# Performance work log

Measured on AMD Instinct MI355X. Metric: run time of the kernel, lower is better.

Reference implementation:

```python
import math
import jax, jax.numpy as jnp
import numpy as np

RATIO = 0.5
N_CHANNELS = 64
B = 64
N_PER = 8192  # nodes per batch element (equal counts for a regular reference)
D_POS = 3


def setup_inputs() -> dict:
    key = jax.random.key(0)
    k1, k2, k3 = jax.random.split(key, 3)
    N = B * N_PER
    positions = jax.random.normal(k1, (N, D_POS), dtype=jnp.float32)
    weights = jax.random.normal(k2, (N, N_CHANNELS), dtype=jnp.float32)
    w = jax.random.normal(k3, (N_CHANNELS,), dtype=jnp.float32)  # SelectTopK learnable vector
    batch = jnp.full((B,), N_PER, dtype=jnp.int32)  # per-batch-element node counts
    return {"positions": positions, "weights": weights, "w": w, "batch": batch}


def reference(positions, weights, w, batch):
    # SelectTopK: score = tanh((x @ w) / ||w||), then per-batch top-ceil(ratio*n) selection.
    n_b = batch.shape[0]
    n_per = positions.shape[0] // n_b
    k = int(math.ceil(RATIO * n_per))

    score = jnp.tanh((weights @ w) / jnp.linalg.norm(w))          # [N]
    top_vals, top_idx = jax.lax.top_k(score.reshape(n_b, n_per), k)  # [B,k] each

    # global node indices of selected nodes (descending score within each batch element)
    node_index = (top_idx + jnp.arange(n_b, dtype=top_idx.dtype)[:, None] * n_per).reshape(-1)  # [B*k]

    pos_sel = positions[node_index]                               # [B*k, D_POS]
    w_sel = weights[node_index] * top_vals.reshape(-1)[:, None]   # [B*k, C] gated by score
    # histc recount: each batch element keeps exactly k nodes
    new_batch = jnp.full((n_b,), k, dtype=jnp.int32)
    return pos_sel, w_sel, new_batch
```

## Files before the change

kernel.cpp:

```cpp
#include <hip/hip_runtime.h>
#include <math.h>

#define C 64
#define DPOS 3
#define NPER 8192
#define KK 4096
#define IDX_MASK 0x1FFFULL

typedef unsigned long long ull;

__device__ __forceinline__ ull score_key(double s, unsigned idx) {
    ull u = (ull)__double_as_longlong(s);
    ull o = (u >> 63) ? ~u : (u | 0x8000000000000000ULL);
    ull d = ~o;
    return (d & ~IDX_MASK) | (ull)idx;
}

__device__ __forceinline__ float key_to_score(ull key) {
    ull o = ~key;
    ull u = (o >> 63) ? (o & 0x7FFFFFFFFFFFFFFFULL) : ~o;
    u &= ~IDX_MASK;
    return (float)__longlong_as_double((long long)u);
}

__global__ void score_kernel(const float* __restrict__ weights,
                             const float* __restrict__ w,
                             ull* __restrict__ keys, int n) {
    int wid = (blockIdx.x * blockDim.x + threadIdx.x) >> 6;
    int lane = threadIdx.x & 63;
    int c4 = lane & 15;
    float4 wv = ((const float4*)w)[c4];
    double nrm = (double)wv.x * wv.x + (double)wv.y * wv.y +
                 (double)wv.z * wv.z + (double)wv.w * wv.w;
    #pragma unroll
    for (int off = 8; off >= 1; off >>= 1) nrm += __shfl_xor(nrm, off, 16);
    double sq = sqrt(nrm);
    #pragma unroll
    for (int it = 0; it < 4; ++it) {
        int r = wid * 16 + it * 4 + (lane >> 4);
        if (r >= n) return;
        float4 x = ((const float4*)weights)[(size_t)r * 16 + c4];
        double acc = (double)x.x * wv.x + (double)x.y * wv.y +
                     (double)x.z * wv.z + (double)x.w * wv.w;
        #pragma unroll
        for (int off = 8; off >= 1; off >>= 1) acc += __shfl_xor(acc, off, 16);
        double s = tanh(acc / sq);
        if (c4 == 0) keys[r] = score_key(s, (unsigned)(r & (NPER - 1)));
    }
}

#define CH 1024
#define CTH 128
__global__ __launch_bounds__(CTH) void sort_chunk(ull* __restrict__ keys) {
    __shared__ ull lds[CH];
    const int tid = threadIdx.x;
    ull* bk = keys + (size_t)blockIdx.x * CH;
    #pragma unroll
    for (int s = 0; s < CH / CTH; ++s) lds[tid + s * CTH] = bk[tid + s * CTH];
    for (unsigned k = 2; k <= CH; k <<= 1) {
        for (unsigned j = k >> 1; j > 0; j >>= 1) {
            __syncthreads();
            #pragma unroll
            for (int s = 0; s < CH / CTH; ++s) {
                unsigned i = tid + s * CTH;
                unsigned ixj = i ^ j;
                if (ixj > i) {
                    ull a = lds[i], b = lds[ixj];
                    bool up = ((i & k) == 0);
                    if ((a > b) == up) { lds[i] = b; lds[ixj] = a; }
                }
            }
        }
    }
    __syncthreads();
    #pragma unroll
    for (int s = 0; s < CH / CTH; ++s) bk[tid + s * CTH] = lds[tid + s * CTH];
}

__global__ void merge_kernel(const ull* __restrict__ src, ull* __restrict__ dst,
                             int L, int outLen, int nPairs) {
    const int T = 8;
    long long ob = ((long long)blockIdx.x * blockDim.x + threadIdx.x) * T;
    if (ob >= (long long)nPairs * outLen) return;
    int pair = (int)(ob / outLen);
    int o = (int)(ob % outLen);
    const ull* A = src + (size_t)pair * (2 * L);
    const ull* B = A + L;
    ull* Cp = dst + (size_t)pair * (2 * L);
    int lo = o - L; if (lo < 0) lo = 0;
    int hi = o < L ? o : L;
    while (lo < hi) {
        int m = (lo + hi) >> 1;
        if (A[m] < B[o - 1 - m]) lo = m + 1; else hi = m;
    }
    int a = lo, b = o - lo;
    ull va = (a < L) ? A[a] : ~0ULL;
    ull vb = (b < L) ? B[b] : ~0ULL;
    #pragma unroll
    for (int t = 0; t < T; ++t) {
        bool fromA = va < vb;
        Cp[o + t] = fromA ? va : vb;
        if (fromA) { ++a; va = (a < L) ? A[a] : ~0ULL; }
        else       { ++b; vb = (b < L) ? B[b] : ~0ULL; }
    }
}

__global__ __launch_bounds__(1024) void sort_full(ull* __restrict__ keys) {
    __shared__ ull lds[NPER];
    const unsigned tid = threadIdx.x;
    ull* bk = keys + (size_t)blockIdx.x * NPER;
    #pragma unroll
    for (int s = 0; s < NPER / 1024; ++s) lds[tid + s * 1024] = bk[tid + s * 1024];
    for (unsigned k = 2; k <= NPER; k <<= 1) {
        for (unsigned j = k >> 1; j > 0; j >>= 1) {
            __syncthreads();
            #pragma unroll
            for (int s = 0; s < NPER / 1024; ++s) {
                unsigned i = tid + s * 1024;
                unsigned ixj = i ^ j;
                if (ixj > i) {
                    ull a = lds[i], b = lds[ixj];
                    bool up = ((i & k) == 0);
                    if ((a > b) == up) { lds[i] = b; lds[ixj] = a; }
                }
            }
        }
    }
    __syncthreads();
    #pragma unroll
    for (int s = 0; s < NPER / 1024; ++s) bk[tid + s * 1024] = lds[tid + s * 1024];
}

__global__ void gather_kernel(const float* __restrict__ positions,
                              const float* __restrict__ weights,
                              const ull* __restrict__ keys,
                              float* __restrict__ out_pos,
                              float* __restrict__ out_w,
                              float* __restrict__ out_batch,
                              int rows, int nb) {
    int gid = blockIdx.x * blockDim.x + threadIdx.x;
    if (gid < nb) out_batch[gid] = (float)KK;
    int lane = gid & 63;
    int sub = lane >> 4, c4 = lane & 15;
    int r = (gid >> 6) * 4 + sub;
    if (r >= rows) return;
    int b = r >> 12;
    int j = r & (KK - 1);
    ull key = keys[(size_t)b * NPER + j];
    unsigned idx = (unsigned)(key & IDX_MASK);
    size_t node = (size_t)b * NPER + idx;
    float s = key_to_score(key);
    float4 x = ((const float4*)weights)[node * 16 + c4];
    float4 y; y.x = x.x * s; y.y = x.y * s; y.z = x.z * s; y.w = x.w * s;
    ((float4*)out_w)[(size_t)r * 16 + c4] = y;
    if (c4 < DPOS)
        out_pos[(size_t)r * DPOS + c4] = positions[node * DPOS + c4];
}

extern "C" void kernel_launch(void* const* d_in, const int* in_sizes, int n_in,
                              void* d_out, int out_size, void* d_ws, size_t ws_size,
                              hipStream_t stream) {
    const float* positions = (const float*)d_in[0];
    const float* weights   = (const float*)d_in[1];
    const float* w         = (const float*)d_in[2];

    int n  = in_sizes[1] / C;
    int nb = in_sizes[3];
    int rows = nb * KK;

    ull* bufA = (ull*)d_ws;
    ull* bufB = bufA + n;
    bool have_dbuf = ws_size >= (size_t)n * 2 * sizeof(ull);

    score_kernel<<<n / 64, 256, 0, stream>>>(weights, w, bufA, n);

    const ull* sorted_keys;
    if (have_dbuf) {
        sort_chunk<<<n / CH, CTH, 0, stream>>>(bufA);
        merge_kernel<<<(n / 8 + 255) / 256, 256, 0, stream>>>(bufA, bufB, 1024, 2048, n / 2048);
        merge_kernel<<<(n / 8 + 255) / 256, 256, 0, stream>>>(bufB, bufA, 2048, 4096, n / 4096);
        merge_kernel<<<((nb * KK) / 8 + 255) / 256, 256, 0, stream>>>(bufA, bufB, 4096, 4096, nb);
        sorted_keys = bufB;
    } else {
        sort_full<<<nb, 1024, 0, stream>>>(bufA);
        sorted_keys = bufA;
    }

    long long gthreads = (long long)(rows / 4) * 64;
    gather_kernel<<<(int)((gthreads + 255) / 256), 256, 0, stream>>>(
        positions, weights, sorted_keys, (float*)d_out,
        (float*)d_out + (size_t)rows * DPOS,
        (float*)d_out + (size_t)rows * (DPOS + C),
        rows, nb);
}
```

Before: 303.2 us.

## Tile merge passes through LDS and switch score computation to fp32

Merge passes now run as block-level tiled merges: two threads find the merge-path split points for each 1024-element output tile, the block stages the inputs into LDS, merges there, and writes the tile back with coalesced stores. This replaces per-thread global binary searches and scattered global reads. The score kernel moves from double to float arithmetic, and the key packs the float score in the high 32 bits with the index in the low bits, so tie ordering is exact. The last merge writes a compact top-k buffer, and the gather indexes it with a new stride argument. Using fp32 tanh and dot products may reorder near-equal scores compared with the fp64 reference path.

```diff
diff --git a/kernel.cpp b/kernel.cpp
--- a/kernel.cpp
+++ b/kernel.cpp
@@ -5,47 +5,45 @@
 #define DPOS 3
 #define NPER 8192
 #define KK 4096
-#define IDX_MASK 0x1FFFULL
 
 typedef unsigned long long ull;
 
-__device__ __forceinline__ ull score_key(double s, unsigned idx) {
-    ull u = (ull)__double_as_longlong(s);
-    ull o = (u >> 63) ? ~u : (u | 0x8000000000000000ULL);
-    ull d = ~o;
-    return (d & ~IDX_MASK) | (ull)idx;
-}
-
-__device__ __forceinline__ float key_to_score(ull key) {
-    ull o = ~key;
-    ull u = (o >> 63) ? (o & 0x7FFFFFFFFFFFFFFFULL) : ~o;
-    u &= ~IDX_MASK;
-    return (float)__longlong_as_double((long long)u);
-}
-
-__global__ void score_kernel(const float* __restrict__ weights,
-                             const float* __restrict__ w,
-                             ull* __restrict__ keys, int n) {
+__device__ __forceinline__ ull make_key(float s, unsigned idx) {
+    unsigned u = __float_as_uint(s);
+    unsigned o = (u >> 31) ? ~u : (u | 0x80000000u);
+    unsigned d = ~o;
+    return ((ull)d << 32) | (ull)idx;
+}
+__device__ __forceinline__ float key_score(ull key) {
+    unsigned o = ~(unsigned)(key >> 32);
+    unsigned u = (o >> 31) ? (o & 0x7FFFFFFFu) : ~o;
+    return __uint_as_float(u);
+}
+
+__global__ __launch_bounds__(256) void score_kernel(const float* __restrict__ weights,
+                                                    const float* __restrict__ w,
+                                                    ull* __restrict__ keys, int n) {
     int wid = (blockIdx.x * blockDim.x + threadIdx.x) >> 6;
     int lane = threadIdx.x & 63;
-    int c4 = lane & 15;
-    float4 wv = ((const float4*)w)[c4];
-    double nrm = (double)wv.x * wv.x + (double)wv.y * wv.y +
-                 (double)wv.z * wv.z + (double)wv.w * wv.w;
-    #pragma unroll
-    for (int off = 8; off >= 1; off >>= 1) nrm += __shfl_xor(nrm, off, 16);
-    double sq = sqrt(nrm);
+    int c4 = lane & 15, sub = lane >> 4;
+    const float4* wv4 = (const float4*)w;
+    float nrm = 0.f;
+    #pragma unroll
+    for (int i = 0; i < 16; ++i) {
+        float4 t = wv4[i];
+        nrm += t.x * t.x + t.y * t.y + t.z * t.z + t.w * t.w;
+    }
+    float nw = sqrtf(nrm);
+    float4 wv = wv4[c4];
     #pragma unroll
     for (int it = 0; it < 4; ++it) {
-        int r = wid * 16 + it * 4 + (lane >> 4);
-        if (r >= n) return;
+        int r = wid * 16 + it * 4 + sub;
         float4 x = ((const float4*)weights)[(size_t)r * 16 + c4];
-        double acc = (double)x.x * wv.x + (double)x.y * wv.y +
-                     (double)x.z * wv.z + (double)x.w * wv.w;
+        float acc = x.x * wv.x + x.y * wv.y + x.z * wv.z + x.w * wv.w;
         #pragma unroll
         for (int off = 8; off >= 1; off >>= 1) acc += __shfl_xor(acc, off, 16);
-        double s = tanh(acc / sq);
-        if (c4 == 0) keys[r] = score_key(s, (unsigned)(r & (NPER - 1)));
+        if (c4 == 0 && r < n)
+            keys[r] = make_key(tanhf(acc / nw), (unsigned)(r & (NPER - 1)));
     }
 }
 
@@ -77,32 +75,54 @@
     for (int s = 0; s < CH / CTH; ++s) bk[tid + s * CTH] = lds[tid + s * CTH];
 }
 
-__global__ void merge_kernel(const ull* __restrict__ src, ull* __restrict__ dst,
-                             int L, int outLen, int nPairs) {
-    const int T = 8;
-    long long ob = ((long long)blockIdx.x * blockDim.x + threadIdx.x) * T;
-    if (ob >= (long long)nPairs * outLen) return;
-    int pair = (int)(ob / outLen);
-    int o = (int)(ob % outLen);
+#define MT 256
+#define MTILE 1024
+__global__ __launch_bounds__(MT) void merge_tiled(const ull* __restrict__ src,
+                                                  ull* __restrict__ dst,
+                                                  int L, int tilesPerPair, int outStride) {
+    __shared__ ull in[MTILE];
+    __shared__ ull ob[MTILE];
+    __shared__ int sAB[2];
+    int tile = blockIdx.x;
+    int pair = tile / tilesPerPair;
+    int o0 = (tile - pair * tilesPerPair) * MTILE;
     const ull* A = src + (size_t)pair * (2 * L);
     const ull* B = A + L;
-    ull* Cp = dst + (size_t)pair * (2 * L);
-    int lo = o - L; if (lo < 0) lo = 0;
-    int hi = o < L ? o : L;
+    ull* D = dst + (size_t)pair * outStride;
+    int tid = threadIdx.x;
+    if (tid < 2) {
+        int o = o0 + tid * MTILE;
+        int lo = o - L; if (lo < 0) lo = 0;
+        int hi = o < L ? o : L;
+        while (lo < hi) {
+            int m = (lo + hi) >> 1;
+            if (A[m] < B[o - 1 - m]) lo = m + 1; else hi = m;
+        }
+        sAB[tid] = lo;
+    }
+    __syncthreads();
+    int aLo = sAB[0], aHi = sAB[1];
+    int na = aHi - aLo;
+    int bLo = o0 - aLo;
+    int nb2 = MTILE - na;
+    for (int i = tid; i < na; i += MT) in[i] = A[aLo + i];
+    for (int i = tid; i < nb2; i += MT) in[na + i] = B[bLo + i];
+    __syncthreads();
+    int o = tid * 4;
+    int lo = o - nb2; if (lo < 0) lo = 0;
+    int hi = o < na ? o : na;
     while (lo < hi) {
         int m = (lo + hi) >> 1;
-        if (A[m] < B[o - 1 - m]) lo = m + 1; else hi = m;
+        if (in[m] < in[na + o - 1 - m]) lo = m + 1; else hi = m;
     }
     int a = lo, b = o - lo;
-    ull va = (a < L) ? A[a] : ~0ULL;
-    ull vb = (b < L) ? B[b] : ~0ULL;
-    #pragma unroll
-    for (int t = 0; t < T; ++t) {
-        bool fromA = va < vb;
-        Cp[o + t] = fromA ? va : vb;
-        if (fromA) { ++a; va = (a < L) ? A[a] : ~0ULL; }
-        else       { ++b; vb = (b < L) ? B[b] : ~0ULL; }
-    }
+    #pragma unroll
+    for (int t = 0; t < 4; ++t) {
+        bool fromA = (b >= nb2) || (a < na && in[a] < in[na + b]);
+        ob[o + t] = fromA ? in[a++] : in[na + b++];
+    }
+    __syncthreads();
+    for (int i = tid; i < MTILE; i += MT) D[o0 + i] = ob[i];
 }
 
 __global__ __launch_bounds__(1024) void sort_full(ull* __restrict__ keys) {
@@ -131,13 +151,13 @@
     for (int s = 0; s < NPER / 1024; ++s) bk[tid + s * 1024] = lds[tid + s * 1024];
 }
 
-__global__ void gather_kernel(const float* __restrict__ positions,
-                              const float* __restrict__ weights,
-                              const ull* __restrict__ keys,
-                              float* __restrict__ out_pos,
-                              float* __restrict__ out_w,
-                              float* __restrict__ out_batch,
-                              int rows, int nb) {
+__global__ __launch_bounds__(256) void gather_kernel(const float* __restrict__ positions,
+                                                     const float* __restrict__ weights,
+                                                     const ull* __restrict__ keys,
+                                                     float* __restrict__ out_pos,
+                                                     float* __restrict__ out_w,
+                                                     float* __restrict__ out_batch,
+                                                     int rows, int nb, int kstr) {
     int gid = blockIdx.x * blockDim.x + threadIdx.x;
     if (gid < nb) out_batch[gid] = (float)KK;
     int lane = gid & 63;
@@ -146,10 +166,10 @@
     if (r >= rows) return;
     int b = r >> 12;
     int j = r & (KK - 1);
-    ull key = keys[(size_t)b * NPER + j];
-    unsigned idx = (unsigned)(key & IDX_MASK);
-    size_t node = (size_t)b * NPER + idx;
-    float s = key_to_score(key);
+    ull key = keys[(size_t)b * kstr + j];
+    unsigned idx = (unsigned)key;
+    size_t node = ((size_t)b << 13) + idx;
+    float s = key_score(key);
     float4 x = ((const float4*)weights)[node * 16 + c4];
     float4 y; y.x = x.x * s; y.y = x.y * s; y.z = x.z * s; y.w = x.w * s;
     ((float4*)out_w)[(size_t)r * 16 + c4] = y;
@@ -175,15 +195,16 @@
     score_kernel<<<n / 64, 256, 0, stream>>>(weights, w, bufA, n);
 
     const ull* sorted_keys;
+    int kstr;
     if (have_dbuf) {
         sort_chunk<<<n / CH, CTH, 0, stream>>>(bufA);
-        merge_kernel<<<(n / 8 + 255) / 256, 256, 0, stream>>>(bufA, bufB, 1024, 2048, n / 2048);
-        merge_kernel<<<(n / 8 + 255) / 256, 256, 0, stream>>>(bufB, bufA, 2048, 4096, n / 4096);
-        merge_kernel<<<((nb * KK) / 8 + 255) / 256, 256, 0, stream>>>(bufA, bufB, 4096, 4096, nb);
-        sorted_keys = bufB;
+        merge_tiled<<<n / MTILE, MT, 0, stream>>>(bufA, bufB, 1024, 2, 2048);
+        merge_tiled<<<n / MTILE, MT, 0, stream>>>(bufB, bufA, 2048, 4, 4096);
+        merge_tiled<<<(nb * KK) / MTILE, MT, 0, stream>>>(bufA, bufB, 4096, 4, KK);
+        sorted_keys = bufB; kstr = KK;
     } else {
         sort_full<<<nb, 1024, 0, stream>>>(bufA);
-        sorted_keys = bufA;
+        sorted_keys = bufA; kstr = NPER;
     }
 
     long long gthreads = (long long)(rows / 4) * 64;
@@ -191,5 +212,5 @@
         positions, weights, sorted_keys, (float*)d_out,
         (float*)d_out + (size_t)rows * DPOS,
         (float*)d_out + (size_t)rows * (DPOS + C),
-        rows, nb);
-}
+        rows, nb, kstr);
+}
```

After: 301.5 us. About the same (-0.6%).
